# Kernel tuning notes

Hardware: AMD Instinct MI355X
Metric: run time of the kernel (lower is better)

## Reference

```python
import jax, jax.numpy as jnp
import numpy as np

N_NODES = 10000
N_EDGES = 160000
N_GRAPHS = 64
IN_DIM, HID, HEADS, OUT_DIM = 128, 64, 8, 10
NEG_SLOPE = 0.2


def setup_inputs() -> dict:
    key = jax.random.key(0)
    ks = jax.random.split(key, 20)
    x = jax.random.normal(ks[0], (N_NODES, IN_DIM), dtype=jnp.float32)
    edge_index = jax.random.randint(ks[1], (2, N_EDGES), 0, N_NODES, dtype=jnp.int64)
    batch = jnp.sort(jax.random.randint(ks[2], (N_NODES,), 0, N_GRAPHS, dtype=jnp.int64))

    def glorot(k, shape):
        fan_in, fan_out = shape[0], shape[-1]
        lim = jnp.sqrt(6.0 / (fan_in + fan_out)).astype(jnp.float32)
        return jax.random.uniform(k, shape, jnp.float32, -lim, lim)

    d0 = HID * HEADS  # 512
    params = {
        # layer 0: IN_DIM -> HID x HEADS, concat
        'W0': glorot(ks[3], (IN_DIM, HEADS * HID)),
        'asrc0': glorot(ks[4], (HEADS, HID)), 'adst0': glorot(ks[5], (HEADS, HID)),
        'b0': jnp.zeros((HEADS * HID,), jnp.float32),
        # layer 1: 512 -> HID x HEADS, concat
        'W1': glorot(ks[6], (d0, HEADS * HID)),
        'asrc1': glorot(ks[7], (HEADS, HID)), 'adst1': glorot(ks[8], (HEADS, HID)),
        'b1': jnp.zeros((HEADS * HID,), jnp.float32),
        # layer 2: 512 -> HID, heads=1
        'W2': glorot(ks[9], (d0, HID)),
        'asrc2': glorot(ks[10], (1, HID)), 'adst2': glorot(ks[11], (1, HID)),
        'b2': jnp.zeros((HID,), jnp.float32),
        # classifier: 2*HID -> HID -> OUT_DIM
        'cW1': glorot(ks[12], (2 * HID, HID)), 'cb1': jnp.zeros((HID,), jnp.float32),
        'cW2': glorot(ks[13], (HID, OUT_DIM)), 'cb2': jnp.zeros((OUT_DIM,), jnp.float32),
    }
    return {'x': x, 'edge_index': edge_index, 'batch': batch, **params}


def gat_conv(h_in, src, dst, W, a_src, a_dst, b, heads, ch):
    # PyG GATConv (concat=True, negative_slope=0.2), dropout inactive (eval).
    N = h_in.shape[0]
    h = (h_in @ W).reshape(N, heads, ch)                       # [N,H,C]
    a_s = jnp.sum(h * a_src[None], axis=-1)                    # [N,H]
    a_d = jnp.sum(h * a_dst[None], axis=-1)                    # [N,H]
    e = jax.nn.leaky_relu(a_s[src] + a_d[dst], NEG_SLOPE)      # [E,H]
    # per-destination segment softmax (stable)
    m = jax.ops.segment_max(e, dst, num_segments=N)            # [N,H]
    ex = jnp.exp(e - m[dst])
    s = jax.ops.segment_sum(ex, dst, num_segments=N)
    alpha = ex / (s[dst] + 1e-16)                              # [E,H]
    out = jax.ops.segment_sum(h[src] * alpha[:, :, None], dst, num_segments=N)
    return out.reshape(N, heads * ch) + b


def _forward(x, src, dst, batch,
             W0, asrc0, adst0, b0, W1, asrc1, adst1, b1,
             W2, asrc2, adst2, b2, cW1, cb1, cW2, cb2):
    h = gat_conv(x, src, dst, W0, asrc0, adst0, b0, HEADS, HID)
    h = jax.nn.relu(h)
    h = gat_conv(h, src, dst, W1, asrc1, adst1, b1, HEADS, HID)
    h = jax.nn.relu(h)
    h = gat_conv(h, src, dst, W2, asrc2, adst2, b2, 1, HID)    # [N,HID]
    # global mean + max pool over graphs
    sums = jax.ops.segment_sum(h, batch, num_segments=N_GRAPHS)
    cnt = jax.ops.segment_sum(jnp.ones((h.shape[0], 1), h.dtype), batch, num_segments=N_GRAPHS)
    mean = sums / jnp.maximum(cnt, 1.0)
    mx = jax.ops.segment_max(h, batch, num_segments=N_GRAPHS)
    g = jnp.concatenate([mean, mx], axis=1)                    # [G, 2*HID]
    g = jax.nn.relu(g @ cW1 + cb1)
    return g @ cW2 + cb2                                       # [G, OUT_DIM]


def reference(x, edge_index, batch,
              W0, asrc0, adst0, b0, W1, asrc1, adst1, b1,
              W2, asrc2, adst2, b2, cW1, cb1, cW2, cb2):
    # PyG GATConv adds self-loops by default
    loops = jnp.arange(x.shape[0], dtype=edge_index.dtype)
    src = jnp.concatenate([edge_index[0], loops])
    dst = jnp.concatenate([edge_index[1], loops])
    return _forward(x, src, dst, batch,
                    W0, asrc0, adst0, b0, W1, asrc1, adst1, b1,
                    W2, asrc2, adst2, b2, cW1, cb1, cW2, cb2)
```

## Files before the change

### kernel.cpp

```cpp
#include <hip/hip_runtime.h>
#include <hip/hip_bf16.h>
#include <math.h>

#define NN 10000
#define EIN 160000
#define ETOT 170000
#define NG 64
#define INDIM 128
#define HID 64
#define HEADS 8
#define D0 512
#define OUTD 10

using bfrag = __attribute__((ext_vector_type(8))) short;
using ffrag = __attribute__((ext_vector_type(4))) float;

__device__ inline float bf2f(unsigned short u) { return __uint_as_float(((unsigned)u) << 16); }
__device__ inline unsigned short f2bf(float f) {
    __hip_bfloat16 b = __float2bfloat16(f);
    return *reinterpret_cast<unsigned short*>(&b);
}

__device__ void transpose_tile(const float* __restrict__ src, __hip_bfloat16* __restrict__ dst,
                               int R, int C, int bx, int by) {
    __shared__ float tile[32][33];
    int cb = bx * 32, rb = by * 32;
    int tx = threadIdx.x & 31, ty = threadIdx.x >> 5;
#pragma unroll
    for (int i = 0; i < 32; i += 8) {
        int r = rb + ty + i, c = cb + tx;
        tile[ty + i][tx] = (r < R && c < C) ? src[(size_t)r * C + c] : 0.f;
    }
    __syncthreads();
#pragma unroll
    for (int i = 0; i < 32; i += 8) {
        int c = cb + ty + i, r = rb + tx;
        if (c < C && r < R) dst[(size_t)c * R + r] = __float2bfloat16(tile[tx][ty + i]);
    }
}

__global__ __launch_bounds__(256) void prep_kernel(const float* __restrict__ x,
                                                   const float* __restrict__ W0,
                                                   const float* __restrict__ W1,
                                                   const float* __restrict__ W2,
                                                   __hip_bfloat16* __restrict__ xb,
                                                   __hip_bfloat16* __restrict__ W0T,
                                                   __hip_bfloat16* __restrict__ W1T,
                                                   __hip_bfloat16* __restrict__ W2T) {
    int bid = blockIdx.x;
    if (bid < 5000) {
        int i = bid * 256 + threadIdx.x;
        xb[i] = __float2bfloat16(x[i]);
    } else if (bid < 5064) {
        int lb = bid - 5000;
        transpose_tile(W0, W0T, INDIM, D0, lb & 15, lb >> 4);
    } else if (bid < 5320) {
        int lb = bid - 5064;
        transpose_tile(W1, W1T, D0, D0, lb & 15, lb >> 4);
    } else {
        int lb = bid - 5320;
        transpose_tile(W2, W2T, D0, 64, lb & 1, lb >> 1);
    }
}

__global__ void count_kernel(const int* __restrict__ ei, int* __restrict__ cnt) {
    int i = blockIdx.x * 256 + threadIdx.x;
    if (i >= ETOT) return;
    int dst = (i < EIN) ? ei[EIN + i] : (i - EIN);
    atomicAdd(&cnt[dst], 1);
}

__global__ __launch_bounds__(1024) void scan_kernel(const int* __restrict__ cnt,
                                                    int* __restrict__ row_ptr,
                                                    int* __restrict__ cursor) {
    __shared__ int ssum[1024];
    int t = threadIdx.x;
    const int PER = 10;
    int base = t * PER;
    int loc[PER];
    int s = 0;
#pragma unroll
    for (int i = 0; i < PER; i++) {
        int v = (base + i < NN) ? cnt[base + i] : 0;
        loc[i] = s; s += v;
    }
    ssum[t] = s;
    __syncthreads();
    for (int off = 1; off < 1024; off <<= 1) {
        int v = (t >= off) ? ssum[t - off] : 0;
        __syncthreads();
        ssum[t] += v;
        __syncthreads();
    }
    int bs = (t > 0) ? ssum[t - 1] : 0;
#pragma unroll
    for (int i = 0; i < PER; i++) {
        if (base + i < NN) { int v = bs + loc[i]; row_ptr[base + i] = v; cursor[base + i] = v; }
    }
    if (t == 0) row_ptr[NN] = ssum[1023];
}

__global__ void scatter_kernel(const int* __restrict__ ei, int* __restrict__ cursor,
                               int* __restrict__ col_src) {
    int i = blockIdx.x * 256 + threadIdx.x;
    if (i >= ETOT) return;
    int src, dst;
    if (i < EIN) { src = ei[i]; dst = ei[EIN + i]; }
    else { src = i - EIN; dst = src; }
    int pos = atomicAdd(&cursor[dst], 1);
    col_src[pos] = src;
}

#define GBM 128
#define GBN 128
#define GBK 32
#define LPAD 8

__global__ __launch_bounds__(256) void gemm_attn(const __hip_bfloat16* __restrict__ A,
                                                 const __hip_bfloat16* __restrict__ BT,
                                                 float* __restrict__ C,
                                                 __hip_bfloat16* __restrict__ Cb,
                                                 const float* __restrict__ asrc,
                                                 const float* __restrict__ adst,
                                                 float* __restrict__ a_s,
                                                 float* __restrict__ a_d,
                                                 int H, int M, int N, int K) {
    __shared__ __align__(16) short As[GBM][GBK + LPAD];
    __shared__ __align__(16) short Bs[GBN][GBK + LPAD];
    int tid = threadIdx.x;
    int wid = tid >> 6, lane = tid & 63;
    int wr = wid >> 1, wc = wid & 1;
    int brow = blockIdx.y * GBM, bcol = blockIdx.x * GBN;

    ffrag acc[4][4] = {};

    int srow = tid >> 2;
    int skq  = (tid & 3) * 8;

    int kq = (lane >> 4) * 8;
    int ra = lane & 15;

    for (int k0 = 0; k0 < K; k0 += GBK) {
#pragma unroll
        for (int p = 0; p < 2; ++p) {
            int r = srow + p * 64;
            int gr = brow + r;
            bfrag va = {0,0,0,0,0,0,0,0};
            if (gr < M) va = *(const bfrag*)(A + (size_t)gr * K + k0 + skq);
            *(bfrag*)&As[r][skq] = va;
            int gc = bcol + r;
            bfrag vb = {0,0,0,0,0,0,0,0};
            if (gc < N) vb = *(const bfrag*)(BT + (size_t)gc * K + k0 + skq);
            *(bfrag*)&Bs[r][skq] = vb;
        }
        __syncthreads();
        bfrag af[4], bf[4];
#pragma unroll
        for (int m = 0; m < 4; ++m) af[m] = *(const bfrag*)&As[wr * 64 + m * 16 + ra][kq];
#pragma unroll
        for (int n = 0; n < 4; ++n) bf[n] = *(const bfrag*)&Bs[wc * 64 + n * 16 + ra][kq];
#pragma unroll
        for (int m = 0; m < 4; ++m)
#pragma unroll
            for (int n = 0; n < 4; ++n)
                acc[m][n] = __builtin_amdgcn_mfma_f32_16x16x32_bf16(af[m], bf[n], acc[m][n], 0, 0, 0);
        __syncthreads();
    }

    int cr = (lane >> 4) * 4;
    int cc = lane & 15;

#pragma unroll
    for (int m = 0; m < 4; ++m) {
#pragma unroll
        for (int n = 0; n < 4; ++n) {
#pragma unroll
            for (int r = 0; r < 4; ++r) {
                int grow = brow + wr * 64 + m * 16 + cr + r;
                int gcol = bcol + wc * 64 + n * 16 + cc;
                if (grow < M && gcol < N) {
                    float v = acc[m][n][r];
                    if (C)  C[(size_t)grow * N + gcol] = v;
                    if (Cb) Cb[(size_t)grow * N + gcol] = __float2bfloat16(v);
                }
            }
        }
    }

    int head = (bcol >> 6) + wc;
    if (head < H) {
        float asl[4], adl[4];
        int cbase = head * 64;
#pragma unroll
        for (int n = 0; n < 4; ++n) {
            asl[n] = asrc[cbase + n * 16 + cc];
            adl[n] = adst[cbase + n * 16 + cc];
        }
#pragma unroll
        for (int m = 0; m < 4; ++m) {
#pragma unroll
            for (int r = 0; r < 4; ++r) {
                float ps = 0.f, pd = 0.f;
#pragma unroll
                for (int n = 0; n < 4; ++n) {
                    float av = acc[m][n][r];
                    ps += av * asl[n];
                    pd += av * adl[n];
                }
#pragma unroll
                for (int o = 1; o < 16; o <<= 1) {
                    ps += __shfl_xor(ps, o);
                    pd += __shfl_xor(pd, o);
                }
                if (cc == 0) {
                    int row = brow + wr * 64 + m * 16 + cr + r;
                    if (row < M) {
                        a_s[(size_t)row * H + head] = ps;
                        a_d[(size_t)row * H + head] = pd;
                    }
                }
            }
        }
    }
}

__global__ __launch_bounds__(256) void gat_agg8(const __hip_bfloat16* __restrict__ h,
                                                const float* __restrict__ a_s,
                                                const float* __restrict__ a_d,
                                                const int* __restrict__ row_ptr,
                                                const int* __restrict__ col_src,
                                                const float* __restrict__ bias,
                                                __hip_bfloat16* __restrict__ out)
{
    int n = blockIdx.x;
    int tid = threadIdx.x;
    int hh = tid >> 5;
    int c0 = tid * 2;
    int r0 = row_ptr[n], r1 = row_ptr[n + 1];
    float ad = a_d[n * 8 + hh];

    float acc0 = 0.f, acc1 = 0.f, ssum = 0.f;
    const unsigned short* hu = (const unsigned short*)h;
    for (int k = r0; k < r1; k += 8) {
        int kk[8]; int s[8]; float av[8]; unsigned v[8];
#pragma unroll
        for (int i = 0; i < 8; ++i) kk[i] = (k + i < r1) ? k + i : r1 - 1;
#pragma unroll
        for (int i = 0; i < 8; ++i) s[i] = col_src[kk[i]];
#pragma unroll
        for (int i = 0; i < 8; ++i) av[i] = a_s[s[i] * 8 + hh];
#pragma unroll
        for (int i = 0; i < 8; ++i) v[i] = *(const unsigned*)(hu + (size_t)s[i] * 512 + c0);
#pragma unroll
        for (int i = 0; i < 8; ++i) {
            float e = av[i] + ad;
            e = e > 0.f ? e : 0.2f * e;
            float al = __expf(e);
            al = (k + i < r1) ? al : 0.f;
            acc0 += al * bf2f((unsigned short)(v[i] & 0xffff));
            acc1 += al * bf2f((unsigned short)(v[i] >> 16));
            ssum += al;
        }
    }
    float inv = 1.f / (ssum + 1e-16f);
    float2 bv = *(const float2*)(bias + c0);
    float o0 = fmaxf(acc0 * inv + bv.x, 0.f);
    float o1 = fmaxf(acc1 * inv + bv.y, 0.f);
    unsigned pk = (unsigned)f2bf(o0) | ((unsigned)f2bf(o1) << 16);
    *(unsigned*)((unsigned short*)out + (size_t)n * 512 + c0) = pk;
}

__global__ __launch_bounds__(256) void gat_agg1(const float* __restrict__ h,
                                                const float* __restrict__ a_s,
                                                const float* __restrict__ a_d,
                                                const int* __restrict__ row_ptr,
                                                const int* __restrict__ col_src,
                                                const float* __restrict__ bias,
                                                float* __restrict__ out) {
    int n = blockIdx.x * 4 + (threadIdx.x >> 6);
    int lane = threadIdx.x & 63;
    if (n >= NN) return;
    int r0 = row_ptr[n], r1 = row_ptr[n + 1];
    float ad = a_d[n];
    float acc = 0.f, ssum = 0.f;
    for (int k = r0; k < r1; k += 8) {
        int kk[8]; int s[8]; float av[8]; float v[8];
#pragma unroll
        for (int i = 0; i < 8; ++i) kk[i] = (k + i < r1) ? k + i : r1 - 1;
#pragma unroll
        for (int i = 0; i < 8; ++i) s[i] = col_src[kk[i]];
#pragma unroll
        for (int i = 0; i < 8; ++i) av[i] = a_s[s[i]];
#pragma unroll
        for (int i = 0; i < 8; ++i) v[i] = h[(size_t)s[i] * 64 + lane];
#pragma unroll
        for (int i = 0; i < 8; ++i) {
            float e = av[i] + ad;
            e = e > 0.f ? e : 0.2f * e;
            float al = __expf(e);
            al = (k + i < r1) ? al : 0.f;
            acc += al * v[i];
            ssum += al;
        }
    }
    out[(size_t)n * 64 + lane] = acc / (ssum + 1e-16f) + bias[lane];
}

__global__ __launch_bounds__(256) void pool_classify(const float* __restrict__ h,
                                                     const int* __restrict__ batch,
                                                     const float* __restrict__ cW1, const float* __restrict__ cb1,
                                                     const float* __restrict__ cW2, const float* __restrict__ cb2,
                                                     float* __restrict__ out) {
    int g = blockIdx.x;
    int tid = threadIdx.x;
    int lane = tid & 63, w = tid >> 6;

    int lo = 0, hi = NN;
    while (lo < hi) { int mid = (lo + hi) >> 1; if (batch[mid] < g) lo = mid + 1; else hi = mid; }
    int s = lo;
    lo = s; hi = NN;
    while (lo < hi) { int mid = (lo + hi) >> 1; if (batch[mid] < g + 1) lo = mid + 1; else hi = mid; }
    int e = lo;

    float sum = 0.f, mx = -1e30f;
    for (int n = s + w; n < e; n += 4) {
        float v = h[(size_t)n * 64 + lane];
        sum += v; mx = fmaxf(mx, v);
    }
    __shared__ float ssum[4][64], smax[4][64];
    __shared__ float gv[128], c1[64];
    ssum[w][lane] = sum; smax[w][lane] = mx;
    __syncthreads();
    if (tid < 64) {
        float s4 = ssum[0][tid] + ssum[1][tid] + ssum[2][tid] + ssum[3][tid];
        float m4 = fmaxf(fmaxf(smax[0][tid], smax[1][tid]), fmaxf(smax[2][tid], smax[3][tid]));
        int cntv = e - s;
        float c = (float)(cntv > 1 ? cntv : 1);
        gv[tid] = s4 / c;
        gv[64 + tid] = m4;
    }
    __syncthreads();
    if (tid < 64) {
        float acc = cb1[tid];
        for (int k = 0; k < 128; k++) acc += gv[k] * cW1[k * 64 + tid];
        c1[tid] = fmaxf(acc, 0.f);
    }
    __syncthreads();
    if (tid < OUTD) {
        float o = cb2[tid];
        for (int k = 0; k < 64; k++) o += c1[k] * cW2[k * OUTD + tid];
        out[g * OUTD + tid] = o;
    }
}

extern "C" void kernel_launch(void* const* d_in, const int* in_sizes, int n_in,
                              void* d_out, int out_size, void* d_ws, size_t ws_size,
                              hipStream_t stream) {
    const float* x     = (const float*)d_in[0];
    const int*   ei    = (const int*)d_in[1];
    const int*   batch = (const int*)d_in[2];
    const float* W0    = (const float*)d_in[3];
    const float* asrc0 = (const float*)d_in[4];
    const float* adst0 = (const float*)d_in[5];
    const float* b0    = (const float*)d_in[6];
    const float* W1    = (const float*)d_in[7];
    const float* asrc1 = (const float*)d_in[8];
    const float* adst1 = (const float*)d_in[9];
    const float* b1    = (const float*)d_in[10];
    const float* W2    = (const float*)d_in[11];
    const float* asrc2 = (const float*)d_in[12];
    const float* adst2 = (const float*)d_in[13];
    const float* b2    = (const float*)d_in[14];
    const float* cW1   = (const float*)d_in[15];
    const float* cb1   = (const float*)d_in[16];
    const float* cW2   = (const float*)d_in[17];
    const float* cb2   = (const float*)d_in[18];
    float* out = (float*)d_out;

    char* ws = (char*)d_ws;
    size_t off = 0;
    auto alloc = [&](size_t bytes) { void* p = ws + off; off += (bytes + 255) & ~(size_t)255; return p; };
    __hip_bfloat16* bufAb = (__hip_bfloat16*)alloc((size_t)NN * D0 * 2);
    __hip_bfloat16* bufBb = (__hip_bfloat16*)alloc((size_t)NN * D0 * 2);
    float* bufC  = (float*)alloc((size_t)NN * 64 * 4);
    float* bufD  = (float*)alloc((size_t)NN * 64 * 4);
    __hip_bfloat16* xb   = (__hip_bfloat16*)alloc((size_t)NN * INDIM * 2);
    __hip_bfloat16* W0T  = (__hip_bfloat16*)alloc((size_t)D0 * INDIM * 2);
    __hip_bfloat16* W1T  = (__hip_bfloat16*)alloc((size_t)D0 * D0 * 2);
    __hip_bfloat16* W2T  = (__hip_bfloat16*)alloc((size_t)64 * D0 * 2);
    float* a_s     = (float*)alloc((size_t)NN * HEADS * 4);
    float* a_d     = (float*)alloc((size_t)NN * HEADS * 4);
    int*   cnt     = (int*)alloc((size_t)NN * 4);
    int*   row_ptr = (int*)alloc((size_t)(NN + 1) * 4);
    int*   cursor  = (int*)alloc((size_t)NN * 4);
    int*   col_src = (int*)alloc((size_t)(ETOT + 8) * 4);
    (void)ws_size; (void)n_in; (void)in_sizes; (void)out_size;

    prep_kernel<<<5352, 256, 0, stream>>>(x, W0, W1, W2, xb, W0T, W1T, W2T);

    hipMemsetAsync(cnt, 0, (size_t)NN * 4, stream);
    count_kernel<<<(ETOT + 255) / 256, 256, 0, stream>>>(ei, cnt);
    scan_kernel<<<1, 1024, 0, stream>>>(cnt, row_ptr, cursor);
    scatter_kernel<<<(ETOT + 255) / 256, 256, 0, stream>>>(ei, cursor, col_src);

    dim3 gg8(D0 / GBN, (NN + GBM - 1) / GBM);
    dim3 gg1(1, (NN + GBM - 1) / GBM);

    gemm_attn<<<gg8, 256, 0, stream>>>(xb, W0T, nullptr, bufAb, asrc0, adst0, a_s, a_d, HEADS, NN, D0, INDIM);
    gat_agg8<<<NN, 256, 0, stream>>>(bufAb, a_s, a_d, row_ptr, col_src, b0, bufBb);

    gemm_attn<<<gg8, 256, 0, stream>>>(bufBb, W1T, nullptr, bufAb, asrc1, adst1, a_s, a_d, HEADS, NN, D0, D0);
    gat_agg8<<<NN, 256, 0, stream>>>(bufAb, a_s, a_d, row_ptr, col_src, b1, bufBb);

    gemm_attn<<<gg1, 256, 0, stream>>>(bufBb, W2T, bufC, nullptr, asrc2, adst2, a_s, a_d, 1, NN, 64, D0);
    gat_agg1<<<(NN + 3) / 4, 256, 0, stream>>>(bufC, a_s, a_d, row_ptr, col_src, b2, bufD);

    pool_classify<<<NG, 256, 0, stream>>>(bufD, batch, cW1, cb1, cW2, cb2, out);
}
```

Baseline: 194.1 us.

## Share per-edge attention weights via LDS in gat_agg8 and fold count zeroing into prep

The 8-head aggregation kernel now computes each edge's source index and the attention exponent for all 8 heads cooperatively, in batches of 32 edges stored in shared memory. Previously every thread loaded col_src and a_s and computed exp redundantly for each edge. The trade is two barriers per batch. Separately, zeroing the count buffer moves into extra blocks of the prep kernel, which removes a hipMemsetAsync launch.

```diff
diff --git a/kernel.cpp b/kernel.cpp
--- a/kernel.cpp
+++ b/kernel.cpp
@@ -46,7 +46,8 @@
                                                    __hip_bfloat16* __restrict__ xb,
                                                    __hip_bfloat16* __restrict__ W0T,
                                                    __hip_bfloat16* __restrict__ W1T,
-                                                   __hip_bfloat16* __restrict__ W2T) {
+                                                   __hip_bfloat16* __restrict__ W2T,
+                                                   int* __restrict__ cnt) {
     int bid = blockIdx.x;
     if (bid < 5000) {
         int i = bid * 256 + threadIdx.x;
@@ -57,9 +58,12 @@
     } else if (bid < 5320) {
         int lb = bid - 5064;
         transpose_tile(W1, W1T, D0, D0, lb & 15, lb >> 4);
-    } else {
+    } else if (bid < 5352) {
         int lb = bid - 5320;
         transpose_tile(W2, W2T, D0, 64, lb & 1, lb >> 1);
+    } else {
+        int i = (bid - 5352) * 256 + threadIdx.x;
+        if (i < NN) cnt[i] = 0;
     }
 }
 
@@ -237,32 +241,47 @@
     int hh = tid >> 5;
     int c0 = tid * 2;
     int r0 = row_ptr[n], r1 = row_ptr[n + 1];
-    float ad = a_d[n * 8 + hh];
-
-    float acc0 = 0.f, acc1 = 0.f, ssum = 0.f;
+
+    __shared__ float ad_sh[8];
+    __shared__ float al_sh[32][8];
+    __shared__ int   src_sh[32];
+    if (tid < 8) ad_sh[tid] = a_d[n * 8 + tid];
+
+    float acc0 = 0.f, acc1 = 0.f, ss = 0.f;
     const unsigned short* hu = (const unsigned short*)h;
-    for (int k = r0; k < r1; k += 8) {
-        int kk[8]; int s[8]; float av[8]; unsigned v[8];
-#pragma unroll
-        for (int i = 0; i < 8; ++i) kk[i] = (k + i < r1) ? k + i : r1 - 1;
-#pragma unroll
-        for (int i = 0; i < 8; ++i) s[i] = col_src[kk[i]];
-#pragma unroll
-        for (int i = 0; i < 8; ++i) av[i] = a_s[s[i] * 8 + hh];
-#pragma unroll
-        for (int i = 0; i < 8; ++i) v[i] = *(const unsigned*)(hu + (size_t)s[i] * 512 + c0);
-#pragma unroll
-        for (int i = 0; i < 8; ++i) {
-            float e = av[i] + ad;
+
+    for (int kb = r0; kb < r1; kb += 32) {
+        __syncthreads();
+        {
+            int eb = tid >> 3, h8 = tid & 7;
+            int k = kb + eb;
+            int kc = (k < r1) ? k : r1 - 1;
+            int s = col_src[kc];
+            if (h8 == 0) src_sh[eb] = s;
+            float e = a_s[s * 8 + h8] + ad_sh[h8];
             e = e > 0.f ? e : 0.2f * e;
             float al = __expf(e);
-            al = (k + i < r1) ? al : 0.f;
-            acc0 += al * bf2f((unsigned short)(v[i] & 0xffff));
-            acc1 += al * bf2f((unsigned short)(v[i] >> 16));
-            ssum += al;
-        }
-    }
-    float inv = 1.f / (ssum + 1e-16f);
+            al_sh[eb][h8] = (k < r1) ? al : 0.f;
+        }
+        __syncthreads();
+        int nb = (r1 - kb < 32) ? (r1 - kb) : 32;
+        for (int j = 0; j < nb; j += 8) {
+            int s[8]; float al[8]; unsigned v[8];
+#pragma unroll
+            for (int i = 0; i < 8; ++i) s[i] = src_sh[j + i];
+#pragma unroll
+            for (int i = 0; i < 8; ++i) al[i] = al_sh[j + i][hh];
+#pragma unroll
+            for (int i = 0; i < 8; ++i) v[i] = *(const unsigned*)(hu + (size_t)s[i] * 512 + c0);
+#pragma unroll
+            for (int i = 0; i < 8; ++i) {
+                acc0 += al[i] * bf2f((unsigned short)(v[i] & 0xffff));
+                acc1 += al[i] * bf2f((unsigned short)(v[i] >> 16));
+                ss += al[i];
+            }
+        }
+    }
+    float inv = 1.f / (ss + 1e-16f);
     float2 bv = *(const float2*)(bias + c0);
     float o0 = fmaxf(acc0 * inv + bv.x, 0.f);
     float o1 = fmaxf(acc1 * inv + bv.y, 0.f);
@@ -396,9 +415,8 @@
     int*   col_src = (int*)alloc((size_t)(ETOT + 8) * 4);
     (void)ws_size; (void)n_in; (void)in_sizes; (void)out_size;
 
-    prep_kernel<<<5352, 256, 0, stream>>>(x, W0, W1, W2, xb, W0T, W1T, W2T);
-
-    hipMemsetAsync(cnt, 0, (size_t)NN * 4, stream);
+    prep_kernel<<<5392, 256, 0, stream>>>(x, W0, W1, W2, xb, W0T, W1T, W2T, cnt);
+
     count_kernel<<<(ETOT + 255) / 256, 256, 0, stream>>>(ei, cnt);
     scan_kernel<<<1, 1024, 0, stream>>>(cnt, row_ptr, cursor);
     scatter_kernel<<<(ETOT + 255) / 256, 256, 0, stream>>>(ei, cursor, col_src);
```

New measurement: 185.9 us. 1.04x faster.
